# Optimization experiments

Measured on AMD Instinct MI355X. Metric: run time of the kernel, lower is better.

The kernel has to match this reference:

```python
import jax, jax.numpy as jnp
import numpy as np

N_NODES = 40000
N_EDGES = 640000
NFEAT = 256
NHID = 128


def setup_inputs() -> dict:
    key = jax.random.key(0)
    k1, k2, k3, k4 = jax.random.split(key, 4)
    x = jax.random.normal(k1, (N_NODES, NFEAT), dtype=jnp.float32)
    edge_index = jax.random.randint(k2, (2, N_EDGES), 0, N_NODES, dtype=jnp.int64)
    edge_weight = jax.random.uniform(k3, (N_EDGES,), dtype=jnp.float32)
    # Glorot-style init for the GraphConvolution weight, zero bias
    W = jax.random.normal(k4, (NFEAT, NHID), dtype=jnp.float32) * (1.0 / np.sqrt(NFEAT))
    b = jnp.zeros((NHID,), dtype=jnp.float32)
    return {"x": x, "edge_index": edge_index, "edge_weight": edge_weight, "W": W, "b": b}


def reference(x, edge_index, edge_weight, W, b):
    # GraphConvolution: support = x @ W ; out = spmm(adj, support) + b ; relu
    support = x @ W                                   # [N, nhid]
    src, dst = edge_index[0], edge_index[1]
    msgs = support[src] * edge_weight[:, None]        # [E, nhid] gathered messages
    agg = jax.ops.segment_sum(msgs, dst, num_segments=N_NODES)  # [N, nhid]
    return jax.nn.relu(agg + b)
```

## Files before the change

kernel.cpp:

```cpp
#include <hip/hip_runtime.h>

#define NNODES 40000
#define NEDGES 640000
#define NFEAT  256
#define NHID   128

#define RSHIFT 7
#define RNODES 128
#define NR     313
#define CAPR   3000
#define PARTB  250
#define EPB    2560
#define GEMM_BLOCKS (NNODES / 64)

#define SUP_OFF  0u
#define WT_OFF   10240000u
#define RC_OFF   10305536u
#define EBIN_OFF 10307584u
#define WS_NEEDED 18145536u

typedef float floatx4 __attribute__((ext_vector_type(4)));
typedef __bf16 bf16x8 __attribute__((ext_vector_type(8)));
typedef unsigned short ushort8 __attribute__((ext_vector_type(8)));
union BfFrag { ushort8 s; bf16x8 b; };

__device__ __forceinline__ unsigned short f2bf(float f) {
    unsigned int u = __float_as_uint(f);
    u = (u + 0x7FFFu + ((u >> 16) & 1u)) >> 16;
    return (unsigned short)u;
}

__device__ __forceinline__ float4 bf4(unsigned int lo, unsigned int hi) {
    float4 v;
    v.x = __uint_as_float(lo << 16);
    v.y = __uint_as_float(lo & 0xFFFF0000u);
    v.z = __uint_as_float(hi << 16);
    v.w = __uint_as_float(hi & 0xFFFF0000u);
    return v;
}

__global__ __launch_bounds__(256) void setup_wt_cur(const float* __restrict__ W,
                                                    unsigned short* __restrict__ Wt,
                                                    unsigned int* __restrict__ range_cursor) {
    const int i = blockIdx.x * 256 + threadIdx.x;
    if (i < NR) range_cursor[i] = 0;
    if (i < NFEAT * NHID) {
        const int h = i >> 8;
        const int k = i & 255;
        Wt[i] = f2bf(W[k * NHID + h]);
    }
}

__global__ __launch_bounds__(256) void gemm_fill(const float* __restrict__ x,
                                                 const unsigned short* __restrict__ Wt,
                                                 unsigned short* __restrict__ support,
                                                 const int* __restrict__ ei,
                                                 const float* __restrict__ ew,
                                                 unsigned int* __restrict__ range_cursor,
                                                 unsigned long long* __restrict__ ebin) {
    const int tid = threadIdx.x;

    if (blockIdx.x >= GEMM_BLOCKS) {
        __shared__ unsigned int hist[320];
        __shared__ unsigned int sA[320], sB[320];
        __shared__ unsigned int lstart[320];
        __shared__ unsigned int gbase[320];
        __shared__ unsigned int ldscur[320];
        __shared__ unsigned long long recbuf[EPB];
        __shared__ unsigned short rbuf[EPB];

        const int pb   = blockIdx.x - GEMM_BLOCKS;
        const int base = pb * EPB + tid;

        for (int i = tid; i < 320; i += 256) { hist[i] = 0; ldscur[i] = 0; }
        __syncthreads();

        int dst[10];
        #pragma unroll
        for (int j = 0; j < 10; j++) dst[j] = ei[NEDGES + base + j * 256];
        #pragma unroll
        for (int j = 0; j < 10; j++) atomicAdd(&hist[dst[j] >> RSHIFT], 1u);
        __syncthreads();

        for (int i = tid; i < 320; i += 256) sA[i] = (i > 0) ? hist[i - 1] : 0u;
        __syncthreads();
        unsigned int* cur = sA;
        unsigned int* nxt = sB;
        for (int off = 1; off < 320; off <<= 1) {
            for (int i = tid; i < 320; i += 256)
                nxt[i] = cur[i] + ((i >= off) ? cur[i - off] : 0u);
            __syncthreads();
            unsigned int* t = cur; cur = nxt; nxt = t;
        }
        for (int i = tid; i < 320; i += 256) {
            lstart[i] = cur[i];
            gbase[i]  = (i < NR && hist[i] > 0u)
                        ? atomicAdd(&range_cursor[i], hist[i]) : 0u;
        }
        __syncthreads();

        int src[10];
        float w[10];
        #pragma unroll
        for (int j = 0; j < 10; j++) {
            src[j] = ei[base + j * 256];
            w[j]   = ew[base + j * 256];
        }
        #pragma unroll
        for (int j = 0; j < 10; j++) {
            const int r  = dst[j] >> RSHIFT;
            const unsigned int lr = atomicAdd(&ldscur[r], 1u);
            const unsigned int pos = lstart[r] + lr;
            recbuf[pos] = ((unsigned long long)f2bf(w[j]) << 32)
                        | ((unsigned long long)(dst[j] & (RNODES - 1)) << 16)
                        | (unsigned long long)(unsigned int)src[j];
            rbuf[pos] = (unsigned short)r;
        }
        __syncthreads();

        for (int i = tid; i < EPB; i += 256) {
            const int r = rbuf[i];
            const unsigned int slot = gbase[r] + ((unsigned int)i - lstart[r]);
            if (slot < CAPR)
                ebin[(size_t)r * CAPR + slot] = recbuf[i];
        }
        return;
    }

    const int lane = tid & 63;
    const int wv   = tid >> 6;
    const int m    = lane & 15;
    const int quad = lane >> 4;
    const int node = blockIdx.x * 64 + wv * 16 + m;

    BfFrag afrag[8];
    const float* xrow = x + (size_t)node * NFEAT + quad * 8;
    #pragma unroll
    for (int ks = 0; ks < 8; ks++) {
        float4 f0 = *(const float4*)(xrow + ks * 32);
        float4 f1 = *(const float4*)(xrow + ks * 32 + 4);
        afrag[ks].s[0] = f2bf(f0.x); afrag[ks].s[1] = f2bf(f0.y);
        afrag[ks].s[2] = f2bf(f0.z); afrag[ks].s[3] = f2bf(f0.w);
        afrag[ks].s[4] = f2bf(f1.x); afrag[ks].s[5] = f2bf(f1.y);
        afrag[ks].s[6] = f2bf(f1.z); afrag[ks].s[7] = f2bf(f1.w);
    }

    floatx4 acc[8];
    #pragma unroll
    for (int nt = 0; nt < 8; nt++) acc[nt] = (floatx4){0.f, 0.f, 0.f, 0.f};

    #pragma unroll
    for (int nt = 0; nt < 8; nt++) {
        const unsigned short* wrow = Wt + (size_t)(nt * 16 + m) * NFEAT + quad * 8;
        #pragma unroll
        for (int ks = 0; ks < 8; ks++) {
            BfFrag bfrag;
            bfrag.s = *(const ushort8*)(wrow + ks * 32);
            acc[nt] = __builtin_amdgcn_mfma_f32_16x16x32_bf16(afrag[ks].b, bfrag.b,
                                                              acc[nt], 0, 0, 0);
        }
    }

    const int row0 = blockIdx.x * 64 + wv * 16 + quad * 4;
    #pragma unroll
    for (int nt = 0; nt < 8; nt++) {
        #pragma unroll
        for (int r = 0; r < 4; r++) {
            support[(size_t)(row0 + r) * NHID + nt * 16 + m] = f2bf(acc[nt][r]);
        }
    }
}

__global__ __launch_bounds__(512) void gather_range(
        const unsigned int* __restrict__ range_cursor,
        const unsigned long long* __restrict__ ebin,
        const unsigned short* __restrict__ support,
        const float* __restrict__ b,
        float* __restrict__ out) {
    __shared__ unsigned long long srec[CAPR];
    __shared__ unsigned int hcnt[RNODES];
    __shared__ unsigned int hstart[RNODES + 1];
    __shared__ unsigned int sA[RNODES], sB[RNODES];

    const int r   = blockIdx.x;
    const int tid = threadIdx.x;

    unsigned int cnt = range_cursor[r];
    if (cnt > CAPR) cnt = CAPR;
    const unsigned long long* bin = ebin + (size_t)r * CAPR;

    if (tid < RNODES) hcnt[tid] = 0u;
    __syncthreads();

    for (unsigned int i = tid; i < cnt; i += 512)
        atomicAdd(&hcnt[(unsigned int)(bin[i] >> 16) & (RNODES - 1)], 1u);
    __syncthreads();

    if (tid < RNODES) sA[tid] = (tid > 0) ? hcnt[tid - 1] : 0u;
    __syncthreads();
    unsigned int* cur = sA;
    unsigned int* nxt = sB;
    for (int off = 1; off < RNODES; off <<= 1) {
        if (tid < RNODES) nxt[tid] = cur[tid] + ((tid >= off) ? cur[tid - off] : 0u);
        __syncthreads();
        unsigned int* t = cur; cur = nxt; nxt = t;
    }
    if (tid < RNODES) { hstart[tid] = cur[tid]; hcnt[tid] = cur[tid]; }
    if (tid == 0) hstart[RNODES] = cnt;
    __syncthreads();

    for (unsigned int i = tid; i < cnt; i += 512) {
        const unsigned long long rec = bin[i];
        const unsigned int dl = (unsigned int)(rec >> 16) & (RNODES - 1);
        const unsigned int p  = atomicAdd(&hcnt[dl], 1u);
        srec[p] = rec;
    }
    __syncthreads();

    const int nl = tid >> 2;
    const int j  = tid & 3;
    const unsigned int kb = hstart[nl];
    const unsigned int ke = hstart[nl + 1];

    float acc[32];
    #pragma unroll
    for (int t = 0; t < 32; t++) acc[t] = 0.f;

    const uint4* sup4 = (const uint4*)support;
    #pragma unroll 2
    for (unsigned int k = kb; k < ke; ++k) {
        const unsigned long long rec = srec[k];
        const float w  = __uint_as_float(((unsigned int)(rec >> 32)) << 16);
        const int   sc = (int)(rec & 0xFFFFu);
        const uint4* rowp = sup4 + (size_t)sc * 16 + (j << 2);
        const uint4 u0 = rowp[0];
        const uint4 u1 = rowp[1];
        const uint4 u2 = rowp[2];
        const uint4 u3 = rowp[3];
        float4 v;
        v = bf4(u0.x, u0.y); acc[0] += w*v.x;  acc[1] += w*v.y;  acc[2] += w*v.z;  acc[3] += w*v.w;
        v = bf4(u0.z, u0.w); acc[4] += w*v.x;  acc[5] += w*v.y;  acc[6] += w*v.z;  acc[7] += w*v.w;
        v = bf4(u1.x, u1.y); acc[8] += w*v.x;  acc[9] += w*v.y;  acc[10] += w*v.z; acc[11] += w*v.w;
        v = bf4(u1.z, u1.w); acc[12] += w*v.x; acc[13] += w*v.y; acc[14] += w*v.z; acc[15] += w*v.w;
        v = bf4(u2.x, u2.y); acc[16] += w*v.x; acc[17] += w*v.y; acc[18] += w*v.z; acc[19] += w*v.w;
        v = bf4(u2.z, u2.w); acc[20] += w*v.x; acc[21] += w*v.y; acc[22] += w*v.z; acc[23] += w*v.w;
        v = bf4(u3.x, u3.y); acc[24] += w*v.x; acc[25] += w*v.y; acc[26] += w*v.z; acc[27] += w*v.w;
        v = bf4(u3.z, u3.w); acc[28] += w*v.x; acc[29] += w*v.y; acc[30] += w*v.z; acc[31] += w*v.w;
    }

    const int node = r * RNODES + nl;
    if (node < NNODES) {
        const float4* b4p = (const float4*)b + (j << 3);
        float4*       o4  = (float4*)out + (size_t)node * (NHID / 4) + (j << 3);
        #pragma unroll
        for (int t = 0; t < 8; t++) {
            float4 bb = b4p[t];
            float4 v;
            v.x = fmaxf(acc[t * 4 + 0] + bb.x, 0.f);
            v.y = fmaxf(acc[t * 4 + 1] + bb.y, 0.f);
            v.z = fmaxf(acc[t * 4 + 2] + bb.z, 0.f);
            v.w = fmaxf(acc[t * 4 + 3] + bb.w, 0.f);
            o4[t] = v;
        }
    }
}

__global__ __launch_bounds__(256) void gemm_xw(const float* __restrict__ x,
                                               const float* __restrict__ W,
                                               float* __restrict__ support) {
    __shared__ float xs[64 * NFEAT];
    const int tid   = threadIdx.x;
    const int node0 = blockIdx.x * 64;

    const float4* xg  = (const float4*)(x + (size_t)node0 * NFEAT);
    float4*       xs4 = (float4*)xs;
    #pragma unroll
    for (int i = tid; i < 64 * (NFEAT / 4); i += 256) xs4[i] = xg[i];
    __syncthreads();

    const int hg = tid & 31;
    const int ng = tid >> 5;
    const float4* W4 = (const float4*)W;

    float4 acc[8];
    #pragma unroll
    for (int n = 0; n < 8; n++) acc[n] = make_float4(0.f, 0.f, 0.f, 0.f);

    #pragma unroll 4
    for (int k = 0; k < NFEAT; k++) {
        float4 w = W4[k * (NHID / 4) + hg];
        #pragma unroll
        for (int n = 0; n < 8; n++) {
            float xv = xs[(ng * 8 + n) * NFEAT + k];
            acc[n].x = fmaf(xv, w.x, acc[n].x);
            acc[n].y = fmaf(xv, w.y, acc[n].y);
            acc[n].z = fmaf(xv, w.z, acc[n].z);
            acc[n].w = fmaf(xv, w.w, acc[n].w);
        }
    }

    float4* out4 = (float4*)support;
    #pragma unroll
    for (int n = 0; n < 8; n++)
        out4[(size_t)(node0 + ng * 8 + n) * (NHID / 4) + hg] = acc[n];
}

__global__ __launch_bounds__(256) void scatter_edges(const int* __restrict__ ei,
                                                     const float* __restrict__ ew,
                                                     const float* __restrict__ support,
                                                     float* __restrict__ out) {
    const int tid  = threadIdx.x;
    const int lane = tid & 31;
    const int e    = blockIdx.x * 8 + (tid >> 5);
    const int   src = ei[e];
    const int   dst = ei[NEDGES + e];
    const float w   = ew[e];
    const float4* s4 = (const float4*)support;
    float4 v = s4[(size_t)src * (NHID / 4) + lane];
    float* o = out + (size_t)dst * NHID + lane * 4;
    atomicAdd(o + 0, v.x * w);
    atomicAdd(o + 1, v.y * w);
    atomicAdd(o + 2, v.z * w);
    atomicAdd(o + 3, v.w * w);
}

__global__ __launch_bounds__(256) void finalize(float* __restrict__ out,
                                                const float* __restrict__ b) {
    const int i = blockIdx.x * 256 + threadIdx.x;
    float4*       o4 = (float4*)out;
    const float4* b4 = (const float4*)b;
    float4 v  = o4[i];
    float4 bb = b4[i & 31];
    v.x = fmaxf(v.x + bb.x, 0.f);
    v.y = fmaxf(v.y + bb.y, 0.f);
    v.z = fmaxf(v.z + bb.z, 0.f);
    v.w = fmaxf(v.w + bb.w, 0.f);
    o4[i] = v;
}

extern "C" void kernel_launch(void* const* d_in, const int* in_sizes, int n_in,
                              void* d_out, int out_size, void* d_ws, size_t ws_size,
                              hipStream_t stream) {
    const float* x  = (const float*)d_in[0];
    const int*   ei = (const int*)d_in[1];
    const float* ew = (const float*)d_in[2];
    const float* W  = (const float*)d_in[3];
    const float* b  = (const float*)d_in[4];
    float*       out = (float*)d_out;

    char* ws = (char*)d_ws;

    if (ws_size >= WS_NEEDED) {
        unsigned short*     support = (unsigned short*)(ws + SUP_OFF);
        unsigned short*     Wt      = (unsigned short*)(ws + WT_OFF);
        unsigned int*       rcur    = (unsigned int*)(ws + RC_OFF);
        unsigned long long* ebin    = (unsigned long long*)(ws + EBIN_OFF);

        setup_wt_cur<<<160, 256, 0, stream>>>(W, Wt, rcur);
        gemm_fill<<<GEMM_BLOCKS + PARTB, 256, 0, stream>>>(
            x, Wt, support, ei, ew, rcur, ebin);
        gather_range<<<NR, 512, 0, stream>>>(rcur, ebin, support, b, out);
    } else {
        float* support = (float*)(ws + SUP_OFF);
        gemm_xw<<<NNODES / 64, 256, 0, stream>>>(x, W, support);
        hipMemsetAsync(d_out, 0, (size_t)out_size * sizeof(float), stream);
        scatter_edges<<<NEDGES / 8, 256, 0, stream>>>(ei, ew, support, out);
        finalize<<<out_size / 4 / 256, 256, 0, stream>>>(out, b);
    }
}
```

Before: 157.8 us.

## Replace global-cursor edge binning with fixed-capacity per-partition slots

The partition blocks no longer build a shared-memory histogram, run a prefix scan and take global atomics on a per-range cursor. Instead each block writes records directly into a fixed 32-slot bucket per (range, partition) and stores a per-bucket count. The gather kernel has 250 threads each walk one bucket to build the per-node histogram and the compacted shared buffer. This removes global atomics, the intra-block scan and the staging pass. The cost is a much larger, sparsely filled edge buffer, scattered 8-byte writes, and silent drops if any bucket gets more than 32 edges.

```diff
diff --git a/kernel.cpp b/kernel.cpp
--- a/kernel.cpp
+++ b/kernel.cpp
@@ -10,14 +10,16 @@
 #define NR     313
 #define CAPR   3000
 #define PARTB  250
+#define EPT    10
 #define EPB    2560
+#define CAPB   32
 #define GEMM_BLOCKS (NNODES / 64)
 
 #define SUP_OFF  0u
 #define WT_OFF   10240000u
-#define RC_OFF   10305536u
-#define EBIN_OFF 10307584u
-#define WS_NEEDED 18145536u
+#define CNT_OFF  10305536u
+#define EBIN_OFF 10465536u
+#define WS_NEEDED (EBIN_OFF + (size_t)NR * PARTB * CAPB * 8)
 
 typedef float floatx4 __attribute__((ext_vector_type(4)));
 typedef __bf16 bf16x8 __attribute__((ext_vector_type(8)));
@@ -39,16 +41,12 @@
     return v;
 }
 
-__global__ __launch_bounds__(256) void setup_wt_cur(const float* __restrict__ W,
-                                                    unsigned short* __restrict__ Wt,
-                                                    unsigned int* __restrict__ range_cursor) {
+__global__ __launch_bounds__(256) void setup_wt(const float* __restrict__ W,
+                                                unsigned short* __restrict__ Wt) {
     const int i = blockIdx.x * 256 + threadIdx.x;
-    if (i < NR) range_cursor[i] = 0;
-    if (i < NFEAT * NHID) {
-        const int h = i >> 8;
-        const int k = i & 255;
-        Wt[i] = f2bf(W[k * NHID + h]);
-    }
+    const int h = i >> 8;
+    const int k = i & 255;
+    Wt[i] = f2bf(W[k * NHID + h]);
 }
 
 __global__ __launch_bounds__(256) void gemm_fill(const float* __restrict__ x,
@@ -56,73 +54,45 @@
                                                  unsigned short* __restrict__ support,
                                                  const int* __restrict__ ei,
                                                  const float* __restrict__ ew,
-                                                 unsigned int* __restrict__ range_cursor,
+                                                 unsigned short* __restrict__ cnt,
                                                  unsigned long long* __restrict__ ebin) {
     const int tid = threadIdx.x;
 
     if (blockIdx.x >= GEMM_BLOCKS) {
-        __shared__ unsigned int hist[320];
-        __shared__ unsigned int sA[320], sB[320];
-        __shared__ unsigned int lstart[320];
-        __shared__ unsigned int gbase[320];
         __shared__ unsigned int ldscur[320];
-        __shared__ unsigned long long recbuf[EPB];
-        __shared__ unsigned short rbuf[EPB];
-
         const int pb   = blockIdx.x - GEMM_BLOCKS;
         const int base = pb * EPB + tid;
 
-        for (int i = tid; i < 320; i += 256) { hist[i] = 0; ldscur[i] = 0; }
+        for (int i = tid; i < 320; i += 256) ldscur[i] = 0u;
         __syncthreads();
 
-        int dst[10];
-        #pragma unroll
-        for (int j = 0; j < 10; j++) dst[j] = ei[NEDGES + base + j * 256];
-        #pragma unroll
-        for (int j = 0; j < 10; j++) atomicAdd(&hist[dst[j] >> RSHIFT], 1u);
+        int src[EPT], dst[EPT];
+        float w[EPT];
+        #pragma unroll
+        for (int j = 0; j < EPT; j++) {
+            const int e = base + j * 256;
+            src[j] = ei[e];
+            dst[j] = ei[NEDGES + e];
+            w[j]   = ew[e];
+        }
+        #pragma unroll
+        for (int j = 0; j < EPT; j++) {
+            const int r = dst[j] >> RSHIFT;
+            const unsigned int idx = atomicAdd(&ldscur[r], 1u);
+            if (idx < CAPB) {
+                const unsigned long long rec =
+                    ((unsigned long long)f2bf(w[j]) << 32)
+                  | ((unsigned long long)(dst[j] & (RNODES - 1)) << 16)
+                  | (unsigned long long)(unsigned int)src[j];
+                ebin[((size_t)r * PARTB + pb) * CAPB + idx] = rec;
+            }
+        }
         __syncthreads();
 
-        for (int i = tid; i < 320; i += 256) sA[i] = (i > 0) ? hist[i - 1] : 0u;
-        __syncthreads();
-        unsigned int* cur = sA;
-        unsigned int* nxt = sB;
-        for (int off = 1; off < 320; off <<= 1) {
-            for (int i = tid; i < 320; i += 256)
-                nxt[i] = cur[i] + ((i >= off) ? cur[i - off] : 0u);
-            __syncthreads();
-            unsigned int* t = cur; cur = nxt; nxt = t;
-        }
-        for (int i = tid; i < 320; i += 256) {
-            lstart[i] = cur[i];
-            gbase[i]  = (i < NR && hist[i] > 0u)
-                        ? atomicAdd(&range_cursor[i], hist[i]) : 0u;
-        }
-        __syncthreads();
-
-        int src[10];
-        float w[10];
-        #pragma unroll
-        for (int j = 0; j < 10; j++) {
-            src[j] = ei[base + j * 256];
-            w[j]   = ew[base + j * 256];
-        }
-        #pragma unroll
-        for (int j = 0; j < 10; j++) {
-            const int r  = dst[j] >> RSHIFT;
-            const unsigned int lr = atomicAdd(&ldscur[r], 1u);
-            const unsigned int pos = lstart[r] + lr;
-            recbuf[pos] = ((unsigned long long)f2bf(w[j]) << 32)
-                        | ((unsigned long long)(dst[j] & (RNODES - 1)) << 16)
-                        | (unsigned long long)(unsigned int)src[j];
-            rbuf[pos] = (unsigned short)r;
-        }
-        __syncthreads();
-
-        for (int i = tid; i < EPB; i += 256) {
-            const int r = rbuf[i];
-            const unsigned int slot = gbase[r] + ((unsigned int)i - lstart[r]);
-            if (slot < CAPR)
-                ebin[(size_t)r * CAPR + slot] = recbuf[i];
+        for (int i = tid; i < NR; i += 256) {
+            unsigned int c = ldscur[i];
+            if (c > CAPB) c = CAPB;
+            cnt[(size_t)pb * NR + i] = (unsigned short)c;
         }
         return;
     }
@@ -172,7 +142,7 @@
 }
 
 __global__ __launch_bounds__(512) void gather_range(
-        const unsigned int* __restrict__ range_cursor,
+        const unsigned short* __restrict__ cnt,
         const unsigned long long* __restrict__ ebin,
         const unsigned short* __restrict__ support,
         const float* __restrict__ b,
@@ -185,15 +155,18 @@
     const int r   = blockIdx.x;
     const int tid = threadIdx.x;
 
-    unsigned int cnt = range_cursor[r];
-    if (cnt > CAPR) cnt = CAPR;
-    const unsigned long long* bin = ebin + (size_t)r * CAPR;
-
+    unsigned int c_t = 0;
+    const unsigned long long* seg =
+        ebin + ((size_t)r * PARTB + (tid < PARTB ? tid : 0)) * CAPB;
+    if (tid < PARTB) {
+        c_t = cnt[(size_t)tid * NR + r];
+        if (c_t > CAPB) c_t = CAPB;
+    }
     if (tid < RNODES) hcnt[tid] = 0u;
     __syncthreads();
 
-    for (unsigned int i = tid; i < cnt; i += 512)
-        atomicAdd(&hcnt[(unsigned int)(bin[i] >> 16) & (RNODES - 1)], 1u);
+    for (unsigned int k = 0; k < c_t; ++k)
+        atomicAdd(&hcnt[(unsigned int)(seg[k] >> 16) & (RNODES - 1)], 1u);
     __syncthreads();
 
     if (tid < RNODES) sA[tid] = (tid > 0) ? hcnt[tid - 1] : 0u;
@@ -205,22 +178,26 @@
         __syncthreads();
         unsigned int* t = cur; cur = nxt; nxt = t;
     }
-    if (tid < RNODES) { hstart[tid] = cur[tid]; hcnt[tid] = cur[tid]; }
-    if (tid == 0) hstart[RNODES] = cnt;
-    __syncthreads();
-
-    for (unsigned int i = tid; i < cnt; i += 512) {
-        const unsigned long long rec = bin[i];
+    if (tid < RNODES) hstart[tid] = cur[tid];
+    if (tid == RNODES - 1) hstart[RNODES] = cur[RNODES - 1] + hcnt[RNODES - 1];
+    __syncthreads();
+    if (tid < RNODES) hcnt[tid] = hstart[tid];
+    __syncthreads();
+
+    for (unsigned int k = 0; k < c_t; ++k) {
+        const unsigned long long rec = seg[k];
         const unsigned int dl = (unsigned int)(rec >> 16) & (RNODES - 1);
         const unsigned int p  = atomicAdd(&hcnt[dl], 1u);
-        srec[p] = rec;
+        if (p < CAPR) srec[p] = rec;
     }
     __syncthreads();
 
     const int nl = tid >> 2;
     const int j  = tid & 3;
-    const unsigned int kb = hstart[nl];
-    const unsigned int ke = hstart[nl + 1];
+    unsigned int kb = hstart[nl];
+    unsigned int ke = hstart[nl + 1];
+    if (kb > CAPR) kb = CAPR;
+    if (ke > CAPR) ke = CAPR;
 
     float acc[32];
     #pragma unroll
@@ -353,13 +330,13 @@
     if (ws_size >= WS_NEEDED) {
         unsigned short*     support = (unsigned short*)(ws + SUP_OFF);
         unsigned short*     Wt      = (unsigned short*)(ws + WT_OFF);
-        unsigned int*       rcur    = (unsigned int*)(ws + RC_OFF);
+        unsigned short*     cnt     = (unsigned short*)(ws + CNT_OFF);
         unsigned long long* ebin    = (unsigned long long*)(ws + EBIN_OFF);
 
-        setup_wt_cur<<<160, 256, 0, stream>>>(W, Wt, rcur);
+        setup_wt<<<128, 256, 0, stream>>>(W, Wt);
         gemm_fill<<<GEMM_BLOCKS + PARTB, 256, 0, stream>>>(
-            x, Wt, support, ei, ew, rcur, ebin);
-        gather_range<<<NR, 512, 0, stream>>>(rcur, ebin, support, b, out);
+            x, Wt, support, ei, ew, cnt, ebin);
+        gather_range<<<NR, 512, 0, stream>>>(cnt, ebin, support, b, out);
     } else {
         float* support = (float*)(ws + SUP_OFF);
         gemm_xw<<<NNODES / 64, 256, 0, stream>>>(x, W, support);
```

Result: no change. 156.5 us (-0.8%).
